# Kernel optimization log

Measured on AMD Instinct MI355X. Metric: run time of the kernel, lower is better.

## Reference

```python
import jax, jax.numpy as jnp
import numpy as np

N = 100000
E = 1600000
NEG_SLOPE = 0.2


def _param(key, shape, scale=0.05):
    return jax.random.normal(key, shape, dtype=jnp.float32) * scale


def setup_inputs() -> dict:
    key = jax.random.key(0)
    ks = jax.random.split(key, 16)
    x = jax.random.normal(ks[0], (N, 128), dtype=jnp.float32)
    edge_index = jax.random.randint(ks[1], (2, E), 0, N, dtype=jnp.int64)
    # layer 1: 128 -> (H=2, C=64), concat
    W1 = _param(ks[2], (128, 2 * 64)); a_src1 = _param(ks[3], (2, 64)); a_dst1 = _param(ks[4], (2, 64)); b1 = jnp.zeros((128,), jnp.float32)
    # layer 2: 128 -> (H=2, C=64), concat
    W2 = _param(ks[5], (128, 2 * 64)); a_src2 = _param(ks[6], (2, 64)); a_dst2 = _param(ks[7], (2, 64)); b2 = jnp.zeros((128,), jnp.float32)
    # layer 3: 128 -> (H=1, C=64), mean (concat=False)
    W3 = _param(ks[8], (128, 1 * 64)); a_src3 = _param(ks[9], (1, 64)); a_dst3 = _param(ks[10], (1, 64)); b3 = jnp.zeros((64,), jnp.float32)
    return {"x": x, "edge_index": edge_index,
            "W1": W1, "a_src1": a_src1, "a_dst1": a_dst1, "b1": b1,
            "W2": W2, "a_src2": a_src2, "a_dst2": a_dst2, "b2": b2,
            "W3": W3, "a_src3": a_src3, "a_dst3": a_dst3, "b3": b3}


def gat_layer(x, src, dst, W, a_src, a_dst, b, concat):
    H, C = a_src.shape
    n = x.shape[0]
    h = (x @ W).reshape(n, H, C)                      # [N,H,C]
    # per-node attention logits (avoid [E,H,C] gather for the score step)
    al_s = jnp.sum(h * a_src[None], axis=-1)          # [N,H]
    al_d = jnp.sum(h * a_dst[None], axis=-1)          # [N,H]
    e = al_s[src] + al_d[dst]                         # [E',H]
    e = jnp.where(e > 0, e, NEG_SLOPE * e)            # LeakyReLU(0.2)
    # scatter-softmax over incoming edges per destination node
    m = jax.ops.segment_max(e, dst, num_segments=n)   # [N,H]
    ex = jnp.exp(e - m[dst])
    z = jax.ops.segment_sum(ex, dst, num_segments=n)  # [N,H]
    alpha = ex / z[dst]                               # [E',H]
    msg = h[src] * alpha[:, :, None]                  # [E',H,C]
    out = jax.ops.segment_sum(msg, dst, num_segments=n)  # [N,H,C]
    out = out.reshape(n, H * C) if concat else out.mean(axis=1)
    return out + b


def reference(x, edge_index, W1, a_src1, a_dst1, b1, W2, a_src2, a_dst2, b2, W3, a_src3, a_dst3, b3):
    n = x.shape[0]
    loop = jnp.arange(n, dtype=edge_index.dtype)
    src = jnp.concatenate([edge_index[0], loop])      # add self-loops (PyG default)
    dst = jnp.concatenate([edge_index[1], loop])
    h = gat_layer(x, src, dst, W1, a_src1, a_dst1, b1, True)
    h = jax.nn.relu(h)
    h = gat_layer(h, src, dst, W2, a_src2, a_dst2, b2, True)
    h = jax.nn.relu(h)
    return gat_layer(h, src, dst, W3, a_src3, a_dst3, b3, False)
```

## Files before the change

kernel.cpp:

```cpp
#include <hip/hip_runtime.h>
#include <hip/hip_bf16.h>

#define NEG_SLOPE 0.2f
#define BUK_SHIFT 9
#define BUK_SIZE 512
#define BUK_CAP 16384

typedef unsigned short u16;
typedef __attribute__((ext_vector_type(4))) float f4v;
typedef _Float16 h8 __attribute__((ext_vector_type(8)));

__device__ __forceinline__ u16 f2h_bits(_Float16 h) {
    union { _Float16 f; u16 u; } c;
    c.f = h;
    return c.u;
}


__launch_bounds__(256)
__global__ void k_binscatter(const int* __restrict__ ei, int* g_cnt, int* buckets,
                             int E, int nb) {
    __shared__ int lcnt[256], lbase[256], lcur[256];
    int t = threadIdx.x;
    if (t < nb) {
        lcnt[t] = 0;
        lcur[t] = 0;
    }
    __syncthreads();
    int tile0 = blockIdx.x * 4096;
    int pk[16], bk[16];
#pragma unroll
    for (int k = 0; k < 16; k++) {
        int idx = tile0 + k * 256 + t;
        bk[k] = -1;
        if (idx < E) {
            int s = ei[idx];
            int d = ei[E + idx];
            bk[k] = d >> BUK_SHIFT;
            pk[k] = (s << BUK_SHIFT) | (d & (BUK_SIZE - 1));
            atomicAdd(&lcnt[bk[k]], 1);
        }
    }
    __syncthreads();
    if (t < nb && lcnt[t] > 0) lbase[t] = atomicAdd(&g_cnt[t], lcnt[t]);
    __syncthreads();
#pragma unroll
    for (int k = 0; k < 16; k++) {
        if (bk[k] >= 0) {
            int p = lbase[bk[k]] + atomicAdd(&lcur[bk[k]], 1);
            if (p < BUK_CAP) buckets[(bk[k] << 14) + p] = pk[k];
        }
    }
}

__launch_bounds__(512)
__global__ void k_csr(const int* __restrict__ g_cnt, const int* __restrict__ buckets,
                      int* csr_ptr, int* csr_src, int n, int nb) {
    __shared__ int lcnt[512], lsc[512], lcur[512], bsc[512];
    int b = blockIdx.x;
    int t = threadIdx.x;
    int nodes = min(BUK_SIZE, n - b * BUK_SIZE);
    int cnt = min(g_cnt[b], BUK_CAP);
    const int* bp = &buckets[b << 14];

    int bv = 0;
    if (t < nb) bv = min(g_cnt[t], BUK_CAP) + min(BUK_SIZE, n - t * BUK_SIZE);
    bsc[t] = bv;
    __syncthreads();
    for (int off = 1; off < 512; off <<= 1) {
        int x = (t >= off) ? bsc[t - off] : 0;
        __syncthreads();
        bsc[t] += x;
        __syncthreads();
    }
    int boff = bsc[b] - (cnt + nodes);
    int total = bsc[nb - 1];
    __syncthreads();

    lcnt[t] = 0;
    __syncthreads();
    for (int i = t; i < cnt; i += 512) atomicAdd(&lcnt[bp[i] & (BUK_SIZE - 1)], 1);
    __syncthreads();
    int myc = (t < nodes) ? (lcnt[t] + 1) : 0;
    lsc[t] = myc;
    __syncthreads();
    for (int off = 1; off < 512; off <<= 1) {
        int x = (t >= off) ? lsc[t - off] : 0;
        __syncthreads();
        lsc[t] += x;
        __syncthreads();
    }
    int excl = lsc[t] - myc;
    lcur[t] = excl;
    if (t < nodes) csr_ptr[b * BUK_SIZE + t] = boff + excl;
    if (b == nb - 1 && t == 0) csr_ptr[n] = total;
    __syncthreads();
    for (int i = t; i < cnt; i += 512) {
        int v = bp[i];
        int ld = v & (BUK_SIZE - 1);
        int p = atomicAdd(&lcur[ld], 1);
        csr_src[boff + p] = v >> BUK_SHIFT;
    }
    if (t < nodes) {
        int p = atomicAdd(&lcur[t], 1);
        csr_src[boff + p] = b * BUK_SIZE + t;
    }
}


__global__ void k_wsplit_all(const float* __restrict__ W1, const float* __restrict__ W2,
                             const float* __restrict__ W3, u16* __restrict__ T1h,
                             u16* __restrict__ T1l, u16* __restrict__ T2h,
                             u16* __restrict__ T2l, u16* __restrict__ T3h,
                             u16* __restrict__ T3l, int* __restrict__ g_cnt) {
    int t = blockIdx.x * 256 + threadIdx.x;
    if (t < 256) g_cnt[t] = 0;
    const float* W;
    u16 *Th, *Tl;
    int M, idx;
    if (t < 16384) {
        W = W1; Th = T1h; Tl = T1l; M = 128; idx = t;
    } else if (t < 32768) {
        W = W2; Th = T2h; Tl = T2l; M = 128; idx = t - 16384;
    } else if (t < 40960) {
        W = W3; Th = T3h; Tl = T3l; M = 64; idx = t - 32768;
    } else {
        return;
    }
    int c = idx >> 7, k = idx & 127;
    float v = W[(size_t)k * M + c];
    _Float16 h = (_Float16)v;
    _Float16 l = (_Float16)(v - (float)h);
    int ct = c >> 4, ch = k >> 5, q = (k >> 3) & 3, j = k & 7;
    size_t addr = ((size_t)ct * 4 + ch) * 512 + ((c & 15) + 16 * q) * 8 + j;
    Th[addr] = f2h_bits(h);
    Tl[addr] = f2h_bits(l);
}


__device__ __forceinline__ void load_split_f32(const float* __restrict__ X, int row,
                                               int koff, int N, h8& hi, h8& lo) {
    float v[8];
    if (row < N) {
        float4 a = *(const float4*)&X[(size_t)row * 128 + koff];
        float4 b = *(const float4*)&X[(size_t)row * 128 + koff + 4];
        v[0] = a.x; v[1] = a.y; v[2] = a.z; v[3] = a.w;
        v[4] = b.x; v[5] = b.y; v[6] = b.z; v[7] = b.w;
    } else {
#pragma unroll
        for (int i = 0; i < 8; i++) v[i] = 0.f;
    }
    union { h8 s; _Float16 u[8]; } H, L;
#pragma unroll
    for (int i = 0; i < 8; i++) {
        H.u[i] = (_Float16)v[i];
        L.u[i] = (_Float16)(v[i] - (float)H.u[i]);
    }
    hi = H.s;
    lo = L.s;
}

template <int M, bool FP32X>
__launch_bounds__(256)
__global__ void k_gemm_mfma(const float* __restrict__ Xf, const u16* __restrict__ XH,
                            const u16* __restrict__ WTh, const u16* __restrict__ WTl,
                            const float* __restrict__ asrc, const float* __restrict__ adst,
                            _Float16* __restrict__ Hout, float* __restrict__ als,
                            float* __restrict__ ald, int nrows) {
    const int CT = M / 16;
    const int H = (M == 128) ? 2 : 1;
    int tid = threadIdx.x;
    int wv = tid >> 6, lane = tid & 63;
    int q = lane >> 4, nl = lane & 15;
    int R0 = blockIdx.x * 128 + wv * 32;
    int rt0 = R0 >> 4;

    f4v acc[2][CT];
    f4v z4 = {0.f, 0.f, 0.f, 0.f};
#pragma unroll
    for (int rt = 0; rt < 2; rt++)
#pragma unroll
        for (int ct = 0; ct < CT; ct++) acc[rt][ct] = z4;

#pragma unroll
    for (int ch = 0; ch < 4; ch++) {
        h8 ah0, al0, ah1, al1;
        if (FP32X) {
            int koff = ch * 32 + q * 8;
            load_split_f32(Xf, R0 + nl, koff, nrows, ah0, al0);
            load_split_f32(Xf, R0 + 16 + nl, koff, nrows, ah1, al1);
        } else {
            size_t a0 = ((size_t)rt0 * 4 + ch) * 512 + lane * 8;
            size_t a1 = ((size_t)(rt0 + 1) * 4 + ch) * 512 + lane * 8;
            ah0 = *(const h8*)&XH[a0];
            ah1 = *(const h8*)&XH[a1];
        }
#pragma unroll
        for (int ct = 0; ct < CT; ct++) {
            size_t bb = ((size_t)ct * 4 + ch) * 512 + lane * 8;
            h8 bh = *(const h8*)&WTh[bb];
            h8 bl = *(const h8*)&WTl[bb];
            acc[0][ct] = __builtin_amdgcn_mfma_f32_16x16x32_f16(ah0, bh, acc[0][ct], 0, 0, 0);
            acc[0][ct] = __builtin_amdgcn_mfma_f32_16x16x32_f16(ah0, bl, acc[0][ct], 0, 0, 0);
            acc[1][ct] = __builtin_amdgcn_mfma_f32_16x16x32_f16(ah1, bh, acc[1][ct], 0, 0, 0);
            acc[1][ct] = __builtin_amdgcn_mfma_f32_16x16x32_f16(ah1, bl, acc[1][ct], 0, 0, 0);
            if (FP32X) {
                acc[0][ct] = __builtin_amdgcn_mfma_f32_16x16x32_f16(al0, bh, acc[0][ct], 0, 0, 0);
                acc[1][ct] = __builtin_amdgcn_mfma_f32_16x16x32_f16(al1, bh, acc[1][ct], 0, 0, 0);
            }
        }
    }

    float av[CT], dvv[CT];
#pragma unroll
    for (int ct = 0; ct < CT; ct++) {
        av[ct] = asrc[ct * 16 + nl];
        dvv[ct] = adst[ct * 16 + nl];
    }
    float ps[2][4][2], pd[2][4][2];
#pragma unroll
    for (int rt = 0; rt < 2; rt++)
#pragma unroll
        for (int r = 0; r < 4; r++)
            for (int h = 0; h < 2; h++) ps[rt][r][h] = pd[rt][r][h] = 0.f;
#pragma unroll
    for (int rt = 0; rt < 2; rt++)
#pragma unroll
        for (int ct = 0; ct < CT; ct++) {
            int h = (M == 128) ? (ct >> 2) : 0;
#pragma unroll
            for (int r = 0; r < 4; r++) {
                ps[rt][r][h] = fmaf(acc[rt][ct][r], av[ct], ps[rt][r][h]);
                pd[rt][r][h] = fmaf(acc[rt][ct][r], dvv[ct], pd[rt][r][h]);
            }
        }

#pragma unroll
    for (int rt = 0; rt < 2; rt++)
#pragma unroll
        for (int ct = 0; ct < CT; ct++)
#pragma unroll
            for (int r = 0; r < 4; r++) {
                int row = R0 + rt * 16 + q * 4 + r;
                if (row < nrows) Hout[(size_t)row * M + ct * 16 + nl] = (_Float16)acc[rt][ct][r];
            }

#pragma unroll
    for (int rt = 0; rt < 2; rt++)
#pragma unroll
        for (int r = 0; r < 4; r++)
#pragma unroll
            for (int h = 0; h < H; h++) {
                float v1 = ps[rt][r][h], v2 = pd[rt][r][h];
                for (int m = 1; m <= 8; m <<= 1) {
                    v1 += __shfl_xor(v1, m);
                    v2 += __shfl_xor(v2, m);
                }
                int row = R0 + rt * 16 + q * 4 + r;
                if (nl == 0 && row < nrows) {
                    als[(size_t)row * H + h] = v1;
                    ald[(size_t)row * H + h] = v2;
                }
            }
}


__launch_bounds__(256)
__global__ void k_agg128(const int* __restrict__ ptr, const int* __restrict__ srcv,
                         const _Float16* __restrict__ Hh, const float* __restrict__ als,
                         const float* __restrict__ ald, const float* __restrict__ bias,
                         u16* __restrict__ OutX, int n) {
    int wvg = (blockIdx.x * blockDim.x + threadIdx.x) >> 6;
    int lane = threadIdx.x & 63;
    int nn = lane >> 4;
    int gl = lane & 15;
    int wid = wvg * 4 + nn;
    bool valid = wid < n;
    int widc = valid ? wid : (n - 1);
    int start = ptr[widc];
    int deg = valid ? (ptr[widc + 1] - start) : 0;
    int md = deg;
    md = max(md, __shfl_xor(md, 16));
    md = max(md, __shfl_xor(md, 32));
    float2 adv = *(const float2*)&ald[(size_t)widc * 2];
    int hsel = gl >> 3;
    int coff = gl * 8;
    float z0 = 0.f, z1 = 0.f;
    float acc[8];
#pragma unroll
    for (int c = 0; c < 8; c++) acc[c] = 0.f;

    for (int base = 0; base < md; base += 16) {
        int i = base + gl;
        int s_l = 0;
        float ex0 = 0.f, ex1 = 0.f;
        if (i < deg) {
            s_l = srcv[start + i];
            float2 av = *(const float2*)&als[(size_t)s_l * 2];
            float e0 = av.x + adv.x;
            e0 = e0 > 0.f ? e0 : NEG_SLOPE * e0;
            ex0 = __expf(e0);
            float e1 = av.y + adv.y;
            e1 = e1 > 0.f ? e1 : NEG_SLOPE * e1;
            ex1 = __expf(e1);
        }
        z0 += ex0;
        z1 += ex1;
        int cnt = min(16, md - base);
        for (int jp = 0; jp < cnt; jp += 4) {
            int nk = min(4, cnt - jp);
            h8 hv[4];
            float w[4];
#pragma unroll
            for (int k = 0; k < 4; k++) {
                if (k < nk) {
                    int j = nn * 16 + jp + k;
                    int s = __shfl(s_l, j);
                    float w0 = __shfl(ex0, j);
                    float w1 = __shfl(ex1, j);
                    w[k] = hsel ? w1 : w0;
                    hv[k] = *(const h8*)&Hh[(size_t)s * 128 + coff];
                }
            }
#pragma unroll
            for (int k = 0; k < 4; k++) {
                if (k < nk) {
#pragma unroll
                    for (int c = 0; c < 8; c++)
                        acc[c] = fmaf(w[k], (float)hv[k][c], acc[c]);
                }
            }
        }
    }

#pragma unroll
    for (int m = 1; m <= 8; m <<= 1) {
        z0 += __shfl_xor(z0, m);
        z1 += __shfl_xor(z1, m);
    }
    if (valid) {
        float zinv = hsel ? (1.f / z1) : (1.f / z0);
        float4 b0 = *(const float4*)&bias[coff];
        float4 b1 = *(const float4*)&bias[coff + 4];
        float bb[8] = {b0.x, b0.y, b0.z, b0.w, b1.x, b1.y, b1.z, b1.w};
        union { _Float16 f[8]; h8 v; } O;
#pragma unroll
        for (int c = 0; c < 8; c++) {
            float o = fmaxf(fmaf(acc[c], zinv, bb[c]), 0.f);
            O.f[c] = (_Float16)o;
        }
        int ch = coff >> 5, qq = (coff >> 3) & 3;
        size_t tb = ((size_t)(wid >> 4) * 4 + ch) * 512 + ((size_t)((wid & 15) + 16 * qq)) * 8;
        *(h8*)&OutX[tb] = O.v;
    }
}


__launch_bounds__(256)
__global__ void k_agg64(const int* __restrict__ ptr, const int* __restrict__ srcv,
                        const _Float16* __restrict__ Hh, const float* __restrict__ als,
                        const float* __restrict__ ald, const float* __restrict__ bias,
                        float* __restrict__ Out, int n) {
    int wvg = (blockIdx.x * blockDim.x + threadIdx.x) >> 6;
    int lane = threadIdx.x & 63;
    int nn = lane >> 3;
    int gl = lane & 7;
    int wid = wvg * 8 + nn;
    bool valid = wid < n;
    int widc = valid ? wid : (n - 1);
    int start = ptr[widc];
    int deg = valid ? (ptr[widc + 1] - start) : 0;
    int md = deg;
    md = max(md, __shfl_xor(md, 8));
    md = max(md, __shfl_xor(md, 16));
    md = max(md, __shfl_xor(md, 32));
    float ad0 = ald[widc];
    int coff = gl * 8;
    float z = 0.f;
    float acc[8];
#pragma unroll
    for (int c = 0; c < 8; c++) acc[c] = 0.f;

    for (int base = 0; base < md; base += 8) {
        int i = base + gl;
        int s_l = 0;
        float ex0 = 0.f;
        if (i < deg) {
            s_l = srcv[start + i];
            float e = als[s_l] + ad0;
            e = e > 0.f ? e : NEG_SLOPE * e;
            ex0 = __expf(e);
        }
        z += ex0;
        int cnt = min(8, md - base);
        for (int jp = 0; jp < cnt; jp += 4) {
            int nk = min(4, cnt - jp);
            h8 hv[4];
            float w[4];
#pragma unroll
            for (int k = 0; k < 4; k++) {
                if (k < nk) {
                    int j = nn * 8 + jp + k;
                    int s = __shfl(s_l, j);
                    w[k] = __shfl(ex0, j);
                    hv[k] = *(const h8*)&Hh[(size_t)s * 64 + coff];
                }
            }
#pragma unroll
            for (int k = 0; k < 4; k++) {
                if (k < nk) {
#pragma unroll
                    for (int c = 0; c < 8; c++)
                        acc[c] = fmaf(w[k], (float)hv[k][c], acc[c]);
                }
            }
        }
    }

#pragma unroll
    for (int m = 1; m <= 4; m <<= 1) z += __shfl_xor(z, m);
    if (valid) {
        float zinv = 1.f / z;
        float4 b0 = *(const float4*)&bias[coff];
        float4 b1 = *(const float4*)&bias[coff + 4];
        float4 o1, o2;
        o1.x = fmaf(acc[0], zinv, b0.x);
        o1.y = fmaf(acc[1], zinv, b0.y);
        o1.z = fmaf(acc[2], zinv, b0.z);
        o1.w = fmaf(acc[3], zinv, b0.w);
        o2.x = fmaf(acc[4], zinv, b1.x);
        o2.y = fmaf(acc[5], zinv, b1.y);
        o2.z = fmaf(acc[6], zinv, b1.z);
        o2.w = fmaf(acc[7], zinv, b1.w);
        *(float4*)&Out[(size_t)wid * 64 + coff] = o1;
        *(float4*)&Out[(size_t)wid * 64 + coff + 4] = o2;
    }
}


extern "C" void kernel_launch(void* const* d_in, const int* in_sizes, int n_in,
                              void* d_out, int out_size, void* d_ws, size_t ws_size,
                              hipStream_t stream) {
    const float* x = (const float*)d_in[0];
    const int* ei = (const int*)d_in[1];
    const float* W1 = (const float*)d_in[2];
    const float* as1 = (const float*)d_in[3];
    const float* ad1 = (const float*)d_in[4];
    const float* b1 = (const float*)d_in[5];
    const float* W2 = (const float*)d_in[6];
    const float* as2 = (const float*)d_in[7];
    const float* ad2 = (const float*)d_in[8];
    const float* b2 = (const float*)d_in[9];
    const float* W3 = (const float*)d_in[10];
    const float* as3 = (const float*)d_in[11];
    const float* ad3 = (const float*)d_in[12];
    const float* b3 = (const float*)d_in[13];

    const int N = in_sizes[0] / 128;
    const int E = in_sizes[1] / 2;
    const int NB = (N + BUK_SIZE - 1) / BUK_SIZE;
    const int Npad = (N + 127) & ~127;

    char* p = (char*)d_ws;
    auto alloc = [&](size_t bytes) -> char* {
        char* r = p;
        p += (bytes + 255) & ~(size_t)255;
        return r;
    };
    int* g_cnt = (int*)alloc(256 * 4);
    int* buckets = (int*)alloc((size_t)NB * BUK_CAP * 4);
    int* csr_ptr = (int*)alloc((size_t)(N + 1) * 4);
    int* csr_src = (int*)alloc((size_t)(E + N) * 4);
    float* als = (float*)alloc((size_t)N * 2 * 4);
    float* aldv = (float*)alloc((size_t)N * 2 * 4);
    _Float16* Hbuf = (_Float16*)alloc((size_t)N * 128 * 2);
    u16* XH = (u16*)alloc((size_t)Npad * 128 * 2);
    u16* WT1h = (u16*)alloc(128 * 128 * 2);
    u16* WT1l = (u16*)alloc(128 * 128 * 2);
    u16* WT2h = (u16*)alloc(128 * 128 * 2);
    u16* WT2l = (u16*)alloc(128 * 128 * 2);
    u16* WT3h = (u16*)alloc(128 * 64 * 2);
    u16* WT3l = (u16*)alloc(128 * 64 * 2);

    const int nbG = Npad / 128;
    const int waves128 = (N + 3) / 4;
    const int nbAgg128 = (waves128 + 3) / 4;
    const int waves64 = (N + 7) / 8;
    const int nbAgg64 = (waves64 + 3) / 4;
    const int nbTile = (E + 4095) / 4096;

    k_wsplit_all<<<160, 256, 0, stream>>>(W1, W2, W3, WT1h, WT1l, WT2h, WT2l, WT3h,
                                          WT3l, g_cnt);

    k_binscatter<<<nbTile, 256, 0, stream>>>(ei, g_cnt, buckets, E, NB);
    k_csr<<<NB, 512, 0, stream>>>(g_cnt, buckets, csr_ptr, csr_src, N, NB);

    k_gemm_mfma<128, true><<<nbG, 256, 0, stream>>>(x, nullptr, WT1h, WT1l,
                                                    as1, ad1, Hbuf, als, aldv, N);
    k_agg128<<<nbAgg128, 256, 0, stream>>>(csr_ptr, csr_src, Hbuf, als, aldv, b1, XH, N);

    k_gemm_mfma<128, false><<<nbG, 256, 0, stream>>>(nullptr, XH, WT2h, WT2l,
                                                     as2, ad2, Hbuf, als, aldv, N);
    k_agg128<<<nbAgg128, 256, 0, stream>>>(csr_ptr, csr_src, Hbuf, als, aldv, b2, XH, N);

    k_gemm_mfma<64, false><<<nbG, 256, 0, stream>>>(nullptr, XH, WT3h, WT3l,
                                                    as3, ad3, Hbuf, als, aldv, N);
    k_agg64<<<nbAgg64, 256, 0, stream>>>(csr_ptr, csr_src, Hbuf, als, aldv, b3,
                                         (float*)d_out, N);
}
```

Before: 418.8 us.

## Precompute per-edge source index and exp weight in separate prep kernel

Adds a k_prep kernel that, for every CSR edge, computes the LeakyReLU exp attention weight and writes it next to the source index as an int2 record, one array per head. The aggregation kernels then stream these records with 8 independent loads per iteration and accumulate z per lane, instead of computing exps and broadcasting indices and weights through shuffles. This is meant to expose more memory-level parallelism in the gather loop and remove the shuffle and reduction overhead. In exchange it adds a kernel launch per layer plus writing and reading roughly 8 bytes per edge per head, and the redundant per-lane record loads are served through the cache.

```diff
diff --git a/kernel.cpp b/kernel.cpp
--- a/kernel.cpp
+++ b/kernel.cpp
@@ -265,11 +265,44 @@
 }
 
 
+template <int H>
 __launch_bounds__(256)
-__global__ void k_agg128(const int* __restrict__ ptr, const int* __restrict__ srcv,
-                         const _Float16* __restrict__ Hh, const float* __restrict__ als,
-                         const float* __restrict__ ald, const float* __restrict__ bias,
-                         u16* __restrict__ OutX, int n) {
+__global__ void k_prep(const int* __restrict__ ptr, const int* __restrict__ srcv,
+                       const float* __restrict__ als, const float* __restrict__ ald,
+                       int2* __restrict__ m0, int2* __restrict__ m1, int n) {
+    int t = blockIdx.x * 256 + threadIdx.x;
+    int node = t >> 2, sub = t & 3;
+    if (node >= n) return;
+    int start = ptr[node], end = ptr[node + 1];
+    if (H == 2) {
+        float2 adv = *(const float2*)&ald[(size_t)node * 2];
+        for (int i = start + sub; i < end; i += 4) {
+            int s = srcv[i];
+            float2 av = *(const float2*)&als[(size_t)s * 2];
+            float e0 = av.x + adv.x;
+            e0 = e0 > 0.f ? e0 : NEG_SLOPE * e0;
+            float e1 = av.y + adv.y;
+            e1 = e1 > 0.f ? e1 : NEG_SLOPE * e1;
+            m0[i] = make_int2(s, __float_as_int(__expf(e0)));
+            m1[i] = make_int2(s, __float_as_int(__expf(e1)));
+        }
+    } else {
+        float ad0 = ald[node];
+        for (int i = start + sub; i < end; i += 4) {
+            int s = srcv[i];
+            float e = als[s] + ad0;
+            e = e > 0.f ? e : NEG_SLOPE * e;
+            m0[i] = make_int2(s, __float_as_int(__expf(e)));
+        }
+    }
+}
+
+
+__launch_bounds__(256)
+__global__ void k_agg128(const int* __restrict__ ptr, const int2* __restrict__ m0,
+                         const int2* __restrict__ m1, const _Float16* __restrict__ Hh,
+                         const float* __restrict__ bias, u16* __restrict__ OutX,
+                         int n, int etot) {
     int wvg = (blockIdx.x * blockDim.x + threadIdx.x) >> 6;
     int lane = threadIdx.x & 63;
     int nn = lane >> 4;
@@ -282,64 +315,37 @@
     int md = deg;
     md = max(md, __shfl_xor(md, 16));
     md = max(md, __shfl_xor(md, 32));
-    float2 adv = *(const float2*)&ald[(size_t)widc * 2];
-    int hsel = gl >> 3;
+    const int2* mb = (gl >> 3) ? m1 : m0;
     int coff = gl * 8;
-    float z0 = 0.f, z1 = 0.f;
+    float z = 0.f;
     float acc[8];
 #pragma unroll
     for (int c = 0; c < 8; c++) acc[c] = 0.f;
 
-    for (int base = 0; base < md; base += 16) {
-        int i = base + gl;
-        int s_l = 0;
-        float ex0 = 0.f, ex1 = 0.f;
-        if (i < deg) {
-            s_l = srcv[start + i];
-            float2 av = *(const float2*)&als[(size_t)s_l * 2];
-            float e0 = av.x + adv.x;
-            e0 = e0 > 0.f ? e0 : NEG_SLOPE * e0;
-            ex0 = __expf(e0);
-            float e1 = av.y + adv.y;
-            e1 = e1 > 0.f ? e1 : NEG_SLOPE * e1;
-            ex1 = __expf(e1);
-        }
-        z0 += ex0;
-        z1 += ex1;
-        int cnt = min(16, md - base);
-        for (int jp = 0; jp < cnt; jp += 4) {
-            int nk = min(4, cnt - jp);
-            h8 hv[4];
-            float w[4];
-#pragma unroll
-            for (int k = 0; k < 4; k++) {
-                if (k < nk) {
-                    int j = nn * 16 + jp + k;
-                    int s = __shfl(s_l, j);
-                    float w0 = __shfl(ex0, j);
-                    float w1 = __shfl(ex1, j);
-                    w[k] = hsel ? w1 : w0;
-                    hv[k] = *(const h8*)&Hh[(size_t)s * 128 + coff];
-                }
+    for (int jp = 0; jp < md; jp += 8) {
+        int nk = min(8, md - jp);
+        int2 mv[8];
+#pragma unroll
+        for (int k = 0; k < 8; k++)
+            if (k < nk) mv[k] = mb[min(start + jp + k, etot - 1)];
+        h8 hv[8];
+#pragma unroll
+        for (int k = 0; k < 8; k++)
+            if (k < nk) hv[k] = *(const h8*)&Hh[(size_t)mv[k].x * 128 + coff];
+#pragma unroll
+        for (int k = 0; k < 8; k++) {
+            if (k < nk) {
+                float w = (jp + k < deg) ? __int_as_float(mv[k].y) : 0.f;
+                z += w;
+#pragma unroll
+                for (int c = 0; c < 8; c++)
+                    acc[c] = fmaf(w, (float)hv[k][c], acc[c]);
             }
-#pragma unroll
-            for (int k = 0; k < 4; k++) {
-                if (k < nk) {
-#pragma unroll
-                    for (int c = 0; c < 8; c++)
-                        acc[c] = fmaf(w[k], (float)hv[k][c], acc[c]);
-                }
-            }
-        }
-    }
-
-#pragma unroll
-    for (int m = 1; m <= 8; m <<= 1) {
-        z0 += __shfl_xor(z0, m);
-        z1 += __shfl_xor(z1, m);
-    }
+        }
+    }
+
     if (valid) {
-        float zinv = hsel ? (1.f / z1) : (1.f / z0);
+        float zinv = 1.f / z;
         float4 b0 = *(const float4*)&bias[coff];
         float4 b1 = *(const float4*)&bias[coff + 4];
         float bb[8] = {b0.x, b0.y, b0.z, b0.w, b1.x, b1.y, b1.z, b1.w};
@@ -357,10 +363,9 @@
 
 
 __launch_bounds__(256)
-__global__ void k_agg64(const int* __restrict__ ptr, const int* __restrict__ srcv,
-                        const _Float16* __restrict__ Hh, const float* __restrict__ als,
-                        const float* __restrict__ ald, const float* __restrict__ bias,
-                        float* __restrict__ Out, int n) {
+__global__ void k_agg64(const int* __restrict__ ptr, const int2* __restrict__ m0,
+                        const _Float16* __restrict__ Hh, const float* __restrict__ bias,
+                        float* __restrict__ Out, int n, int etot) {
     int wvg = (blockIdx.x * blockDim.x + threadIdx.x) >> 6;
     int lane = threadIdx.x & 63;
     int nn = lane >> 3;
@@ -374,51 +379,34 @@
     md = max(md, __shfl_xor(md, 8));
     md = max(md, __shfl_xor(md, 16));
     md = max(md, __shfl_xor(md, 32));
-    float ad0 = ald[widc];
     int coff = gl * 8;
     float z = 0.f;
     float acc[8];
 #pragma unroll
     for (int c = 0; c < 8; c++) acc[c] = 0.f;
 
-    for (int base = 0; base < md; base += 8) {
-        int i = base + gl;
-        int s_l = 0;
-        float ex0 = 0.f;
-        if (i < deg) {
-            s_l = srcv[start + i];
-            float e = als[s_l] + ad0;
-            e = e > 0.f ? e : NEG_SLOPE * e;
-            ex0 = __expf(e);
-        }
-        z += ex0;
-        int cnt = min(8, md - base);
-        for (int jp = 0; jp < cnt; jp += 4) {
-            int nk = min(4, cnt - jp);
-            h8 hv[4];
-            float w[4];
-#pragma unroll
-            for (int k = 0; k < 4; k++) {
-                if (k < nk) {
-                    int j = nn * 8 + jp + k;
-                    int s = __shfl(s_l, j);
-                    w[k] = __shfl(ex0, j);
-                    hv[k] = *(const h8*)&Hh[(size_t)s * 64 + coff];
-                }
+    for (int jp = 0; jp < md; jp += 8) {
+        int nk = min(8, md - jp);
+        int2 mv[8];
+#pragma unroll
+        for (int k = 0; k < 8; k++)
+            if (k < nk) mv[k] = m0[min(start + jp + k, etot - 1)];
+        h8 hv[8];
+#pragma unroll
+        for (int k = 0; k < 8; k++)
+            if (k < nk) hv[k] = *(const h8*)&Hh[(size_t)mv[k].x * 64 + coff];
+#pragma unroll
+        for (int k = 0; k < 8; k++) {
+            if (k < nk) {
+                float w = (jp + k < deg) ? __int_as_float(mv[k].y) : 0.f;
+                z += w;
+#pragma unroll
+                for (int c = 0; c < 8; c++)
+                    acc[c] = fmaf(w, (float)hv[k][c], acc[c]);
             }
-#pragma unroll
-            for (int k = 0; k < 4; k++) {
-                if (k < nk) {
-#pragma unroll
-                    for (int c = 0; c < 8; c++)
-                        acc[c] = fmaf(w[k], (float)hv[k][c], acc[c]);
-                }
-            }
-        }
-    }
-
-#pragma unroll
-    for (int m = 1; m <= 4; m <<= 1) z += __shfl_xor(z, m);
+        }
+    }
+
     if (valid) {
         float zinv = 1.f / z;
         float4 b0 = *(const float4*)&bias[coff];
@@ -460,6 +448,7 @@
     const int E = in_sizes[1] / 2;
     const int NB = (N + BUK_SIZE - 1) / BUK_SIZE;
     const int Npad = (N + 127) & ~127;
+    const int ETOT = E + N;
 
     char* p = (char*)d_ws;
     auto alloc = [&](size_t bytes) -> char* {
@@ -470,9 +459,11 @@
     int* g_cnt = (int*)alloc(256 * 4);
     int* buckets = (int*)alloc((size_t)NB * BUK_CAP * 4);
     int* csr_ptr = (int*)alloc((size_t)(N + 1) * 4);
-    int* csr_src = (int*)alloc((size_t)(E + N) * 4);
+    int* csr_src = (int*)alloc((size_t)ETOT * 4);
     float* als = (float*)alloc((size_t)N * 2 * 4);
     float* aldv = (float*)alloc((size_t)N * 2 * 4);
+    int2* meta0 = (int2*)alloc(((size_t)ETOT + 64) * 8);
+    int2* meta1 = (int2*)alloc(((size_t)ETOT + 64) * 8);
     _Float16* Hbuf = (_Float16*)alloc((size_t)N * 128 * 2);
     u16* XH = (u16*)alloc((size_t)Npad * 128 * 2);
     u16* WT1h = (u16*)alloc(128 * 128 * 2);
@@ -488,6 +479,7 @@
     const int waves64 = (N + 7) / 8;
     const int nbAgg64 = (waves64 + 3) / 4;
     const int nbTile = (E + 4095) / 4096;
+    const int nbPrep = (N * 4 + 255) / 256;
 
     k_wsplit_all<<<160, 256, 0, stream>>>(W1, W2, W3, WT1h, WT1l, WT2h, WT2l, WT3h,
                                           WT3l, g_cnt);
@@ -497,14 +489,17 @@
 
     k_gemm_mfma<128, true><<<nbG, 256, 0, stream>>>(x, nullptr, WT1h, WT1l,
                                                     as1, ad1, Hbuf, als, aldv, N);
-    k_agg128<<<nbAgg128, 256, 0, stream>>>(csr_ptr, csr_src, Hbuf, als, aldv, b1, XH, N);
+    k_prep<2><<<nbPrep, 256, 0, stream>>>(csr_ptr, csr_src, als, aldv, meta0, meta1, N);
+    k_agg128<<<nbAgg128, 256, 0, stream>>>(csr_ptr, meta0, meta1, Hbuf, b1, XH, N, ETOT);
 
     k_gemm_mfma<128, false><<<nbG, 256, 0, stream>>>(nullptr, XH, WT2h, WT2l,
                                                      as2, ad2, Hbuf, als, aldv, N);
-    k_agg128<<<nbAgg128, 256, 0, stream>>>(csr_ptr, csr_src, Hbuf, als, aldv, b2, XH, N);
+    k_prep<2><<<nbPrep, 256, 0, stream>>>(csr_ptr, csr_src, als, aldv, meta0, meta1, N);
+    k_agg128<<<nbAgg128, 256, 0, stream>>>(csr_ptr, meta0, meta1, Hbuf, b2, XH, N, ETOT);
 
     k_gemm_mfma<64, false><<<nbG, 256, 0, stream>>>(nullptr, XH, WT3h, WT3l,
                                                     as3, ad3, Hbuf, als, aldv, N);
-    k_agg64<<<nbAgg64, 256, 0, stream>>>(csr_ptr, csr_src, Hbuf, als, aldv, b3,
-                                         (float*)d_out, N);
-}
+    k_prep<1><<<nbPrep, 256, 0, stream>>>(csr_ptr, csr_src, als, aldv, meta0, nullptr, N);
+    k_agg64<<<nbAgg64, 256, 0, stream>>>(csr_ptr, meta0, Hbuf, b3,
+                                         (float*)d_out, N, ETOT);
+}
```

Result: slower. 510.0 us (+21.8%).
